# Performance work log

Hardware: AMD Instinct MI355X
Metric: run time of the kernel (lower is better)

Reference implementation:

```python
import jax, jax.numpy as jnp
import numpy as np

D_MODEL = 1024
N_HEADS = 16
D_K = D_MODEL // N_HEADS
THETA = 10000.0
BATCH, SEQ = 4, 2048


def apply_rope(x, pos, theta=THETA):
    # x: [B, H, S, d_k]; pos: [S] int. Rotate interleaved pairs (x_{2i}, x_{2i+1}).
    half = x.shape[-1] // 2
    inv_freq = theta ** (-jnp.arange(half, dtype=x.dtype) * 2.0 / x.shape[-1])  # [half]
    ang = pos.astype(x.dtype)[:, None] * inv_freq[None, :]                      # [S, half]
    cos, sin = jnp.cos(ang), jnp.sin(ang)
    x1, x2 = x[..., 0::2], x[..., 1::2]
    r1 = x1 * cos - x2 * sin
    r2 = x1 * sin + x2 * cos
    return jnp.stack([r1, r2], axis=-1).reshape(x.shape)


def setup_inputs() -> dict:
    key = jax.random.key(0)
    k1, k2, k3 = jax.random.split(key, 3)
    x = jax.random.normal(k1, (BATCH, SEQ, D_MODEL), dtype=jnp.float32)
    W_qkv = jax.random.normal(k2, (3 * D_MODEL, D_MODEL), dtype=jnp.float32) * (D_MODEL ** -0.5)
    b_qkv = jnp.zeros((3 * D_MODEL,), dtype=jnp.float32)
    W_o = jax.random.normal(k3, (D_MODEL, D_MODEL), dtype=jnp.float32) * (D_MODEL ** -0.5)
    b_o = jnp.zeros((D_MODEL,), dtype=jnp.float32)
    token_positions = jnp.arange(SEQ, dtype=jnp.int64 if jax.config.jax_enable_x64 else jnp.int32)
    return {"x": x, "token_positions": token_positions, "W_qkv": W_qkv,
            "b_qkv": b_qkv, "W_o": W_o, "b_o": b_o}


def reference(x, token_positions, W_qkv, b_qkv, W_o, b_o):
    B, S, _ = x.shape
    qkv = x @ W_qkv.T + b_qkv                                   # [B, S, 3*d_model]
    qkv = qkv.reshape(B, S, 3, N_HEADS, D_K)
    qkv = jnp.transpose(qkv, (2, 0, 3, 1, 4))                   # [3, B, H, S, d_k]
    q, k, v = qkv[0], qkv[1], qkv[2]
    q = apply_rope(q, token_positions)
    k = apply_rope(k, token_positions)
    scores = jnp.einsum('bhqd,bhkd->bhqk', q / jnp.sqrt(jnp.asarray(D_K, x.dtype)), k)
    causal = jnp.tril(jnp.ones((S, S), dtype=bool))             # True where attended
    scores = jnp.where(causal, scores, jnp.asarray(-jnp.inf, scores.dtype))
    attn = jax.nn.softmax(scores, axis=-1)
    out = jnp.einsum('bhqk,bhkd->bhqd', attn, v)                # [B, H, S, d_k]
    out = jnp.transpose(out, (0, 2, 1, 3)).reshape(B, S, D_MODEL)
    return out @ W_o.T + b_o
```

## Files before the change

kernel.cpp:

```cpp
#include <hip/hip_runtime.h>
#include <hip/hip_bf16.h>
#include <cstdint>

#define S_LEN 2048
#define NHEAD 16
#define DMODEL 1024

using short8 = __attribute__((ext_vector_type(8))) short;
using f32x4  = __attribute__((ext_vector_type(4))) float;

__device__ __forceinline__ float bf2f(ushort u) {
    return __uint_as_float(((uint32_t)u) << 16);
}
__device__ __forceinline__ ushort f2bf(float f) {
    uint32_t u = __float_as_uint(f);
    u += 0x7FFF + ((u >> 16) & 1);
    return (ushort)(u >> 16);
}

__global__ void k_cast(const float* __restrict__ in, ushort* __restrict__ out, int n4) {
    int i = blockIdx.x * blockDim.x + threadIdx.x;
    if (i < n4) {
        const float4 v = reinterpret_cast<const float4*>(in)[i];
        ushort4 o;
        o.x = f2bf(v.x); o.y = f2bf(v.y); o.z = f2bf(v.z); o.w = f2bf(v.w);
        reinterpret_cast<ushort4*>(out)[i] = o;
    }
}

__device__ __forceinline__ void gl16(const ushort* g, ushort* l) {
    __builtin_amdgcn_global_load_lds(
        (const __attribute__((address_space(1))) void*)g,
        (__attribute__((address_space(3))) void*)l, 16, 0, 0);
}

template<int OUT_BF16>
__global__ __launch_bounds__(256, 2)
void k_gemm_bt(const ushort* __restrict__ A, const ushort* __restrict__ Bm,
               const float* __restrict__ bias, void* __restrict__ Cout,
               int M, int N, int K)
{
    __shared__ ushort As[128 * 32];
    __shared__ ushort Bs[128 * 32];
    const int t = threadIdx.x;
    const int w = t >> 6, l = t & 63;
    const int lr = l & 15, lg = l >> 4;
    const int bm = blockIdx.y * 128, bn = blockIdx.x * 128;
    const int wr = (w >> 1) * 64, wc = (w & 1) * 64;

    f32x4 acc[4][4] = {};

    const ushort* ag = A + (size_t)(bm + (t >> 2)) * K + (t & 3) * 8;
    const ushort* bg = Bm + (size_t)(bn + (t >> 2)) * K + (t & 3) * 8;
    ushort* asd = &As[t * 8];
    ushort* bsd = &Bs[t * 8];
    const size_t rowskip = (size_t)64 * K;

    for (int k0 = 0; k0 < K; k0 += 32) {
        gl16(ag + k0, asd);
        gl16(ag + rowskip + k0, asd + 2048);
        gl16(bg + k0, bsd);
        gl16(bg + rowskip + k0, bsd + 2048);
        __syncthreads();
        short8 af[4], bf[4];
        #pragma unroll
        for (int m = 0; m < 4; ++m)
            af[m] = *reinterpret_cast<const short8*>(&As[(wr + m * 16 + lr) * 32 + lg * 8]);
        #pragma unroll
        for (int n = 0; n < 4; ++n)
            bf[n] = *reinterpret_cast<const short8*>(&Bs[(wc + n * 16 + lr) * 32 + lg * 8]);
        #pragma unroll
        for (int m = 0; m < 4; ++m)
            #pragma unroll
            for (int n = 0; n < 4; ++n)
                acc[m][n] = __builtin_amdgcn_mfma_f32_16x16x32_bf16(af[m], bf[n], acc[m][n], 0, 0, 0);
        __syncthreads();
    }

    const int col0 = bn + wc + lr;
    float bv[4];
    #pragma unroll
    for (int n = 0; n < 4; ++n) bv[n] = bias[col0 + n * 16];
    #pragma unroll
    for (int m = 0; m < 4; ++m) {
        const int row0 = bm + wr + m * 16 + lg * 4;
        #pragma unroll
        for (int r = 0; r < 4; ++r) {
            const size_t ro = (size_t)(row0 + r) * N;
            #pragma unroll
            for (int n = 0; n < 4; ++n) {
                float v = acc[m][n][r] + bv[n];
                if (OUT_BF16) ((ushort*)Cout)[ro + col0 + n * 16] = f2bf(v);
                else          ((float*)Cout)[ro + col0 + n * 16] = v;
            }
        }
    }
}

__global__ __launch_bounds__(256)
void k_rope_scatter(const ushort* __restrict__ qkv, const int* __restrict__ pos,
                    ushort* __restrict__ Qo, ushort* __restrict__ Ko, ushort* __restrict__ Vt)
{
    __shared__ ushort vlds[64][72];
    const int blk = blockIdx.x;
    const int st = blk & 31, bh = blk >> 5;
    const int b = bh >> 4, h = bh & 15;
    const int t = threadIdx.x;
    const int sl = t >> 2, dc = (t & 3) << 4;
    const int s = st * 64 + sl;
    const size_t base = (size_t)(b * S_LEN + s) * 3072 + h * 64 + dc;
    const float p = (float)pos[s];

    float cs[8], sn[8];
    #pragma unroll
    for (int j = 0; j < 8; ++j) {
        const int fi = (dc >> 1) + j;
        const float invf = __expf(-(float)fi * 0.28782313662425572f);
        __sincosf(p * invf, &sn[j], &cs[j]);
    }

    #pragma unroll
    for (int type = 0; type < 2; ++type) {
        union { uint4 u[2]; ushort us[16]; } in_, out_;
        in_.u[0] = *(const uint4*)(qkv + base + type * 1024);
        in_.u[1] = *(const uint4*)(qkv + base + type * 1024 + 8);
        const float scale = (type == 0) ? 0.125f : 1.0f;
        #pragma unroll
        for (int j = 0; j < 8; ++j) {
            float x1 = bf2f(in_.us[2 * j]), x2 = bf2f(in_.us[2 * j + 1]);
            out_.us[2 * j]     = f2bf((x1 * cs[j] - x2 * sn[j]) * scale);
            out_.us[2 * j + 1] = f2bf((x1 * sn[j] + x2 * cs[j]) * scale);
        }
        ushort* dst = (type == 0 ? Qo : Ko) + ((size_t)(bh * S_LEN + s)) * 64 + dc;
        *(uint4*)dst = out_.u[0];
        *(uint4*)(dst + 8) = out_.u[1];
    }

    {
        uint4 v0 = *(const uint4*)(qkv + base + 2048);
        uint4 v1 = *(const uint4*)(qkv + base + 2048 + 8);
        *(uint4*)&vlds[sl][dc] = v0;
        *(uint4*)&vlds[sl][dc + 8] = v1;
    }
    __syncthreads();
    {
        const int d = t >> 2, sc0 = (t & 3) << 4;
        union { uint4 u[2]; ushort us[16]; } o;
        #pragma unroll
        for (int j = 0; j < 16; ++j) o.us[j] = vlds[sc0 + j][d];
        ushort* dst = Vt + ((size_t)bh * 64 + d) * S_LEN + st * 64 + sc0;
        *(uint4*)dst = o.u[0];
        *(uint4*)(dst + 8) = o.u[1];
    }
}

__global__ __launch_bounds__(256, 3)
void k_attn(const ushort* __restrict__ Q, const ushort* __restrict__ Kk,
            const ushort* __restrict__ Vt, ushort* __restrict__ O)
{
    __shared__ ushort Ks[2][4096];
    __shared__ ushort Vs[2][4096];
    __shared__ ushort P[4][32][80];

    const int blk = blockIdx.x;
    const int qb = 15 - (blk >> 6);
    const int bh = blk & 63;
    const int b = bh >> 4, h = bh & 15;
    const int t = threadIdx.x, w = t >> 6, l = t & 63;
    const int lr = l & 15, lg = l >> 4;

    const ushort* Kb = Kk + (size_t)bh * S_LEN * 64;
    const ushort* Vb = Vt + (size_t)bh * 64 * S_LEN;
    const ushort* Qb = Q + (size_t)bh * S_LEN * 64;

    const int qbase0 = qb * 128 + w * 16;
    const int qbase1 = qbase0 + 64;

    short8 qf[2][2];
    #pragma unroll
    for (int qg = 0; qg < 2; ++qg)
        #pragma unroll
        for (int dh = 0; dh < 2; ++dh)
            qf[qg][dh] = *(const short8*)(Qb + (size_t)(qbase0 + qg * 64 + lr) * 64 + dh * 32 + lg * 8);

    f32x4 acc[2][4] = {};
    float mx[2] = {-INFINITY, -INFINITY}, ls[2] = {0.f, 0.f};

    const int nt = 2 * qb + 2;

    auto stage = [&](int kb2, int buf) {
        ushort* Kd = Ks[buf]; ushort* Vd = Vs[buf];
        #pragma unroll
        for (int j = 0; j < 2; ++j) {
            const int e = (j * 256 + t) * 8;
            const int row = e >> 6;
            const int col = (e & 63) ^ ((row & 7) << 3);
            gl16(Kb + (size_t)(kb2 + row) * 64 + col, Kd + e);
            gl16(Vb + (size_t)row * S_LEN + kb2 + col, Vd + e);
        }
    };

    stage(0, 0);
    __syncthreads();

    for (int kt = 0; kt < nt; ++kt) {
        const int cur = kt & 1;
        const int kb = kt * 64;
        if (kt + 1 < nt) stage(kb + 64, cur ^ 1);

        const ushort* Kl = Ks[cur];
        short8 kf[4][2];
        #pragma unroll
        for (int i = 0; i < 4; ++i) {
            const int krow = i * 16 + lr, sw = (krow & 7) << 3;
            kf[i][0] = *(const short8*)&Kl[krow * 64 + ((lg * 8) ^ sw)];
            kf[i][1] = *(const short8*)&Kl[krow * 64 + ((32 + lg * 8) ^ sw)];
        }

        auto do_group = [&](int qg, int qbaseg, bool domask) {
            f32x4 st[4] = {};
            #pragma unroll
            for (int i = 0; i < 4; ++i) {
                st[i] = __builtin_amdgcn_mfma_f32_16x16x32_bf16(kf[i][0], qf[qg][0], st[i], 0, 0, 0);
                st[i] = __builtin_amdgcn_mfma_f32_16x16x32_bf16(kf[i][1], qf[qg][1], st[i], 0, 0, 0);
            }
            if (domask) {
                const int qrow = qbaseg + lr;
                #pragma unroll
                for (int i = 0; i < 4; ++i)
                    #pragma unroll
                    for (int r = 0; r < 4; ++r)
                        if (kb + i * 16 + lg * 4 + r > qrow) st[i][r] = -INFINITY;
            }
            float tm = st[0][0];
            #pragma unroll
            for (int i = 0; i < 4; ++i)
                #pragma unroll
                for (int r = 0; r < 4; ++r) tm = fmaxf(tm, st[i][r]);
            tm = fmaxf(tm, __shfl_xor(tm, 16));
            tm = fmaxf(tm, __shfl_xor(tm, 32));
            const float mn = fmaxf(mx[qg], tm);
            const float sc = __expf(mx[qg] - mn);
            float ps = 0.f;
            #pragma unroll
            for (int i = 0; i < 4; ++i) {
                ushort4 pv;
                #pragma unroll
                for (int r = 0; r < 4; ++r) {
                    const float e = __expf(st[i][r] - mn);
                    ps += e;
                    ((ushort*)&pv)[r] = f2bf(e);
                }
                *(ushort4*)&P[w][qg * 16 + lr][i * 16 + lg * 4] = pv;
            }
            ps += __shfl_xor(ps, 16);
            ps += __shfl_xor(ps, 32);
            ls[qg] = ls[qg] * sc + ps;
            mx[qg] = mn;
            #pragma unroll
            for (int d = 0; d < 4; ++d)
                #pragma unroll
                for (int r = 0; r < 4; ++r) acc[qg][d][r] *= sc;
        };

        const bool g0 = (kt < nt - 1);
        do_group(1, qbase1, kt == nt - 1);
        if (g0) do_group(0, qbase0, kt == nt - 2);

        short8 pf1[2], pf0[2];
        pf1[0] = *(const short8*)&P[w][16 + lr][lg * 8];
        pf1[1] = *(const short8*)&P[w][16 + lr][32 + lg * 8];
        if (g0) {
            pf0[0] = *(const short8*)&P[w][lr][lg * 8];
            pf0[1] = *(const short8*)&P[w][lr][32 + lg * 8];
        }
        const ushort* Vl = Vs[cur];
        #pragma unroll
        for (int d = 0; d < 4; ++d) {
            const int vrow = d * 16 + lr, sw = (vrow & 7) << 3;
            short8 v0 = *(const short8*)&Vl[vrow * 64 + ((lg * 8) ^ sw)];
            short8 v1 = *(const short8*)&Vl[vrow * 64 + ((32 + lg * 8) ^ sw)];
            acc[1][d] = __builtin_amdgcn_mfma_f32_16x16x32_bf16(v0, pf1[0], acc[1][d], 0, 0, 0);
            acc[1][d] = __builtin_amdgcn_mfma_f32_16x16x32_bf16(v1, pf1[1], acc[1][d], 0, 0, 0);
            if (g0) {
                acc[0][d] = __builtin_amdgcn_mfma_f32_16x16x32_bf16(v0, pf0[0], acc[0][d], 0, 0, 0);
                acc[0][d] = __builtin_amdgcn_mfma_f32_16x16x32_bf16(v1, pf0[1], acc[0][d], 0, 0, 0);
            }
        }
        __syncthreads();
    }

    #pragma unroll
    for (int qg = 0; qg < 2; ++qg) {
        const float inv = 1.f / ls[qg];
        const int q = qbase0 + qg * 64 + lr;
        #pragma unroll
        for (int d = 0; d < 4; ++d) {
            ushort4 ov;
            #pragma unroll
            for (int r = 0; r < 4; ++r) ((ushort*)&ov)[r] = f2bf(acc[qg][d][r] * inv);
            *(ushort4*)&O[((size_t)(b * S_LEN) + q) * 1024 + h * 64 + d * 16 + lg * 4] = ov;
        }
    }
}

extern "C" void kernel_launch(void* const* d_in, const int* in_sizes, int n_in,
                              void* d_out, int out_size, void* d_ws, size_t ws_size,
                              hipStream_t stream)
{
    const float* x    = (const float*)d_in[0];
    const int*   pos  = (const int*)d_in[1];
    const float* Wqkv = (const float*)d_in[2];
    const float* bqkv = (const float*)d_in[3];
    const float* Wo   = (const float*)d_in[4];
    const float* bo   = (const float*)d_in[5];
    float* out = (float*)d_out;

    char* ws = (char*)d_ws;
    ushort* xb   = (ushort*)(ws);
    ushort* wqb  = (ushort*)(ws + 16777216);
    ushort* wob  = (ushort*)(ws + 23068672);
    ushort* qkvb = (ushort*)(ws + 25165824);
    ushort* Qb   = (ushort*)(ws + 75497472);
    ushort* Kb   = (ushort*)(ws + 92274688);
    ushort* Vtb  = (ushort*)(ws + 109051904);
    ushort* AOb  = (ushort*)(ws + 125829120);

    k_cast<<<8192, 256, 0, stream>>>(x, xb, 2097152);
    k_cast<<<3072, 256, 0, stream>>>(Wqkv, wqb, 786432);
    k_cast<<<1024, 256, 0, stream>>>(Wo, wob, 262144);
    k_gemm_bt<1><<<dim3(24, 64), 256, 0, stream>>>(xb, wqb, bqkv, qkvb, 8192, 3072, 1024);
    k_rope_scatter<<<2048, 256, 0, stream>>>(qkvb, pos, Qb, Kb, Vtb);
    k_attn<<<1024, 256, 0, stream>>>(Qb, Kb, Vtb, AOb);
    k_gemm_bt<0><<<dim3(8, 64), 256, 0, stream>>>(AOb, wob, bo, out, 8192, 1024, 1024);
}
```

Measured before the change: 199.1 us.

## Use exp2 softmax with lazy rescaling, packed bf16 converts, and MFMA priority

Folds log2(e) into the Q scale so the softmax can use the raw v_exp_f32 (exp2) instruction directly. It skips the running-max rescale of the accumulator and row sum unless some row's new max exceeds the stored max by more than a threshold of 12 in the log2 domain. Probabilities are packed to bf16 with v_cvt_pk_bf16_f32, and s_setprio is raised around the MFMA blocks to favour matrix issue across waves. The lazy rescale allows unnormalised exponentials up to about 2^12, which is a numeric risk bounded by fp32 and bf16 range.

New measurement: 194.6 us. 1.02x faster.

```diff
diff --git a/kernel.cpp b/kernel.cpp
--- a/kernel.cpp
+++ b/kernel.cpp
@@ -16,6 +16,14 @@
     uint32_t u = __float_as_uint(f);
     u += 0x7FFF + ((u >> 16) & 1);
     return (ushort)(u >> 16);
+}
+__device__ __forceinline__ uint32_t cvt_pk_bf16(float lo, float hi) {
+    uint32_t r;
+    asm("v_cvt_pk_bf16_f32 %0, %1, %2" : "=v"(r) : "v"(lo), "v"(hi));
+    return r;
+}
+__device__ __forceinline__ float exp2_(float x) {
+    float r; asm("v_exp_f32 %0, %1" : "=v"(r) : "v"(x)); return r;
 }
 
 __global__ void k_cast(const float* __restrict__ in, ushort* __restrict__ out, int n4) {
@@ -124,7 +132,7 @@
         union { uint4 u[2]; ushort us[16]; } in_, out_;
         in_.u[0] = *(const uint4*)(qkv + base + type * 1024);
         in_.u[1] = *(const uint4*)(qkv + base + type * 1024 + 8);
-        const float scale = (type == 0) ? 0.125f : 1.0f;
+        const float scale = (type == 0) ? 0.125f * 1.44269504088896f : 1.0f;
         #pragma unroll
         for (int j = 0; j < 8; ++j) {
             float x1 = bf2f(in_.us[2 * j]), x2 = bf2f(in_.us[2 * j + 1]);
@@ -219,11 +227,13 @@
 
         auto do_group = [&](int qg, int qbaseg, bool domask) {
             f32x4 st[4] = {};
+            __builtin_amdgcn_s_setprio(1);
             #pragma unroll
             for (int i = 0; i < 4; ++i) {
                 st[i] = __builtin_amdgcn_mfma_f32_16x16x32_bf16(kf[i][0], qf[qg][0], st[i], 0, 0, 0);
                 st[i] = __builtin_amdgcn_mfma_f32_16x16x32_bf16(kf[i][1], qf[qg][1], st[i], 0, 0, 0);
             }
+            __builtin_amdgcn_s_setprio(0);
             if (domask) {
                 const int qrow = qbaseg + lr;
                 #pragma unroll
@@ -232,35 +242,40 @@
                     for (int r = 0; r < 4; ++r)
                         if (kb + i * 16 + lg * 4 + r > qrow) st[i][r] = -INFINITY;
             }
-            float tm = st[0][0];
-            #pragma unroll
-            for (int i = 0; i < 4; ++i)
-                #pragma unroll
-                for (int r = 0; r < 4; ++r) tm = fmaxf(tm, st[i][r]);
+            float a0 = fmaxf(fmaxf(st[0][0], st[0][1]), fmaxf(st[0][2], st[0][3]));
+            float a1 = fmaxf(fmaxf(st[1][0], st[1][1]), fmaxf(st[1][2], st[1][3]));
+            float a2 = fmaxf(fmaxf(st[2][0], st[2][1]), fmaxf(st[2][2], st[2][3]));
+            float a3 = fmaxf(fmaxf(st[3][0], st[3][1]), fmaxf(st[3][2], st[3][3]));
+            float tm = fmaxf(fmaxf(a0, a1), fmaxf(a2, a3));
             tm = fmaxf(tm, __shfl_xor(tm, 16));
             tm = fmaxf(tm, __shfl_xor(tm, 32));
-            const float mn = fmaxf(mx[qg], tm);
-            const float sc = __expf(mx[qg] - mn);
+            float mn = mx[qg];
+            if (!__all(tm <= mn + 12.0f)) {
+                mn = fmaxf(mx[qg], tm);
+                const float sc = exp2_(mx[qg] - mn);
+                ls[qg] *= sc;
+                #pragma unroll
+                for (int d = 0; d < 4; ++d)
+                    #pragma unroll
+                    for (int r = 0; r < 4; ++r) acc[qg][d][r] *= sc;
+                mx[qg] = mn;
+            }
             float ps = 0.f;
             #pragma unroll
             for (int i = 0; i < 4; ++i) {
-                ushort4 pv;
-                #pragma unroll
-                for (int r = 0; r < 4; ++r) {
-                    const float e = __expf(st[i][r] - mn);
-                    ps += e;
-                    ((ushort*)&pv)[r] = f2bf(e);
-                }
-                *(ushort4*)&P[w][qg * 16 + lr][i * 16 + lg * 4] = pv;
+                const float e0 = exp2_(st[i][0] - mn);
+                const float e1 = exp2_(st[i][1] - mn);
+                const float e2 = exp2_(st[i][2] - mn);
+                const float e3 = exp2_(st[i][3] - mn);
+                ps += (e0 + e1) + (e2 + e3);
+                uint2 pk;
+                pk.x = cvt_pk_bf16(e0, e1);
+                pk.y = cvt_pk_bf16(e2, e3);
+                *(uint2*)&P[w][qg * 16 + lr][i * 16 + lg * 4] = pk;
             }
             ps += __shfl_xor(ps, 16);
             ps += __shfl_xor(ps, 32);
-            ls[qg] = ls[qg] * sc + ps;
-            mx[qg] = mn;
-            #pragma unroll
-            for (int d = 0; d < 4; ++d)
-                #pragma unroll
-                for (int r = 0; r < 4; ++r) acc[qg][d][r] *= sc;
+            ls[qg] += ps;
         };
 
         const bool g0 = (kt < nt - 1);
@@ -275,6 +290,7 @@
             pf0[1] = *(const short8*)&P[w][lr][32 + lg * 8];
         }
         const ushort* Vl = Vs[cur];
+        __builtin_amdgcn_s_setprio(1);
         #pragma unroll
         for (int d = 0; d < 4; ++d) {
             const int vrow = d * 16 + lr, sw = (vrow & 7) << 3;
@@ -287,6 +303,7 @@
                 acc[0][d] = __builtin_amdgcn_mfma_f32_16x16x32_bf16(v1, pf0[1], acc[0][d], 0, 0, 0);
             }
         }
+        __builtin_amdgcn_s_setprio(0);
         __syncthreads();
     }
 
```
